# Performance work log

Measured on AMD Instinct MI355X. Metric: run time of the kernel, lower is better.

Reference implementation:

```python
import jax, jax.numpy as jnp
import numpy as np
import math

H = 8
D_MODEL = 32
D_HEAD = 4
FACTOR = 5
EPS = 1e-5

DATANUM = 1024
B = 512            # outer batch; becomes attention sequence length
C = 32
L = DATANUM // 8   # 128; becomes attention batch
U = min(FACTOR * int(math.ceil(math.log(B))), B)  # 35 (U_part == u since L_Q == L_K == B)


def setup_inputs() -> dict:
    key = jax.random.key(0)
    ks = jax.random.split(key, 16)
    s = 0.05
    return {
        'x': jax.random.normal(ks[0], (B, C, L), jnp.float32),
        'Wq': jax.random.normal(ks[1], (D_MODEL, D_MODEL), jnp.float32) * s,
        'bq': jnp.zeros((D_MODEL,), jnp.float32),
        'Wk': jax.random.normal(ks[2], (D_MODEL, D_MODEL), jnp.float32) * s,
        'bk': jnp.zeros((D_MODEL,), jnp.float32),
        'Wv': jax.random.normal(ks[3], (D_MODEL, D_MODEL), jnp.float32) * s,
        'bv': jnp.zeros((D_MODEL,), jnp.float32),
        'Wo': jax.random.normal(ks[4], (D_MODEL, D_MODEL), jnp.float32) * s,
        'bo': jnp.zeros((D_MODEL,), jnp.float32),
        'bn1_gamma': jnp.ones((C,), jnp.float32),
        'bn1_beta': jnp.zeros((C,), jnp.float32),
        'bn1_mean': jnp.zeros((C,), jnp.float32),
        'bn1_var': jnp.ones((C,), jnp.float32),
        'W1': jax.random.normal(ks[5], (DATANUM * 8, DATANUM * 4), jnp.float32) * 0.01,
        'b1': jnp.zeros((DATANUM * 8,), jnp.float32),
        'W2': jax.random.normal(ks[6], (DATANUM * 4, DATANUM * 8), jnp.float32) * 0.01,
        'b2': jnp.zeros((DATANUM * 4,), jnp.float32),
        'bn2_gamma': jnp.ones((C,), jnp.float32),
        'bn2_beta': jnp.zeros((C,), jnp.float32),
        'bn2_mean': jnp.zeros((C,), jnp.float32),
        'bn2_var': jnp.ones((C,), jnp.float32),
        'index_sample': jax.random.randint(ks[7], (B, U), 0, B, jnp.int64),
    }


def _bn(x, gamma, beta, mean, var):
    # eval-mode BatchNorm1d over channel dim of (batch, C, length)
    inv = jax.lax.rsqrt(var + EPS)
    return (x - mean[None, :, None]) * (inv * gamma)[None, :, None] + beta[None, :, None]


def _prob_attention(Q, K, V, index_sample):
    # Q,K,V: (Ba, H, Lq, D) self-attention, Lq == Lk. Informer ProbAttention, mask_flag=True.
    Ba, Hh, Lq, D = Q.shape
    u = index_sample.shape[1]
    # sparsity measurement on sampled keys
    K_sample = K[:, :, index_sample, :]                       # (Ba,H,Lq,U,D)
    QK_sample = jnp.einsum('bhld,bhlud->bhlu', Q, K_sample)
    M = QK_sample.max(axis=-1) - QK_sample.sum(axis=-1) / Lq  # (Ba,H,Lq)
    _, M_top = jax.lax.top_k(M, u)                            # (Ba,H,u) selected queries
    Q_reduce = jnp.take_along_axis(Q, M_top[..., None], axis=2)  # (Ba,H,u,D)
    scores = jnp.einsum('bhud,bhkd->bhuk', Q_reduce, K) / jnp.sqrt(jnp.float32(D))
    # ProbMask: causal w.r.t. the selected query's original position
    causal = jnp.arange(Lq)[None, None, None, :] > M_top[..., None]
    scores = jnp.where(causal, -jnp.inf, scores)
    attn = jax.nn.softmax(scores, axis=-1)
    upd = jnp.einsum('bhuk,bhkd->bhud', attn, V)              # (Ba,H,u,D)
    context = jnp.cumsum(V, axis=2)                           # initial context (mask_flag=True)
    b_idx = jnp.arange(Ba)[:, None, None]
    h_idx = jnp.arange(Hh)[None, :, None]
    context = context.at[b_idx, h_idx, M_top].set(upd)
    return context


def reference(x, Wq, bq, Wk, bk, Wv, bv, Wo, bo,
              bn1_gamma, bn1_beta, bn1_mean, bn1_var,
              W1, b1, W2, b2,
              bn2_gamma, bn2_beta, bn2_mean, bn2_var,
              index_sample):
    Bsz, Cc, Ll = x.shape
    res1 = x
    xa = jnp.transpose(x, (2, 0, 1))                          # (L, B, 32): attn batch=L, seq=B

    def heads(t):
        return jnp.transpose(t.reshape(Ll, Bsz, H, D_HEAD), (0, 2, 1, 3))

    Q = heads(xa @ Wq.T + bq)
    K = heads(xa @ Wk.T + bk)
    V = heads(xa @ Wv.T + bv)
    ctx = _prob_attention(Q, K, V, index_sample)              # (L,H,B,D)
    out = jnp.transpose(ctx, (0, 2, 1, 3)).reshape(Ll, Bsz, D_MODEL)
    out = out @ Wo.T + bo
    xh = jax.nn.relu(out)                                     # dropout = identity (eval)
    xh = jnp.transpose(xh, (1, 2, 0))                         # (B,32,L)
    xh = _bn(xh + res1, bn1_gamma, bn1_beta, bn1_mean, bn1_var)
    res2 = xh
    f = xh.reshape(Bsz, Cc * Ll)
    f = jax.nn.relu(f @ W1.T + b1)
    f = jax.nn.relu(f @ W2.T + b2)
    f = f.reshape(Bsz, Cc, Ll)
    return _bn(f + res2, bn2_gamma, bn2_beta, bn2_mean, bn2_var)
```

## Files before the change

### kernel.cpp

```cpp
#include <hip/hip_runtime.h>
#include <stdint.h>

#define EPSF 1e-5f
#define NEG_INF (-1e30f)

typedef float f32x4 __attribute__((ext_vector_type(4)));
typedef __bf16 bf16x8 __attribute__((ext_vector_type(8)));
typedef unsigned short u16x8 __attribute__((ext_vector_type(8)));

typedef __attribute__((address_space(3))) unsigned char* as3_ptr;
typedef const __attribute__((address_space(1))) unsigned char* as1_ptr;

__device__ __forceinline__ void async16(const void* g, void* l) {
  __builtin_amdgcn_global_load_lds((as1_ptr)g, (as3_ptr)l, 16, 0, 0);
}

__device__ __forceinline__ unsigned short f2bf(float f) {
  union { float f; unsigned int u; } v; v.f = f;
  unsigned int r = v.u + 0x7FFFu + ((v.u >> 16) & 1u);
  return (unsigned short)(r >> 16);
}
__device__ __forceinline__ unsigned short f2bf_fast(float f) {
  union { float f; unsigned int u; } v; v.f = f;
  return (unsigned short)((v.u + 0x8000u) >> 16);
}

__global__ __launch_bounds__(256) void transpose_k(const float* __restrict__ src,
                                                   float* __restrict__ dst, int R, int C) {
  __shared__ float tl[32][33];
  int tx = threadIdx.x & 31, ty = threadIdx.x >> 5;
  int c0 = blockIdx.x * 32, r0 = blockIdx.y * 32;
#pragma unroll
  for (int i = 0; i < 4; i++)
    tl[ty + i * 8][tx] = src[(size_t)(r0 + ty + i * 8) * C + c0 + tx];
  __syncthreads();
#pragma unroll
  for (int i = 0; i < 4; i++)
    dst[(size_t)(c0 + ty + i * 8) * R + r0 + tx] = tl[tx][ty + i * 8];
}

__global__ __launch_bounds__(256) void qkv_k(const float* __restrict__ xT,
    const float* __restrict__ Wq, const float* __restrict__ bq,
    const float* __restrict__ Wk, const float* __restrict__ bk,
    const float* __restrict__ Wv, const float* __restrict__ bv,
    float* __restrict__ Q, float* __restrict__ Kq, float* __restrict__ Vq) {
  __shared__ float xs[64 * 33];
  __shared__ float wq[32 * 33], wk[32 * 33], wvs[32 * 33];
  __shared__ float bqs[32], bks[32], bvs[32];
  int tid = threadIdx.x;
  int a = blockIdx.x;
  int tbase = blockIdx.y * 256;
#pragma unroll
  for (int i = 0; i < 4; i++) {
    int e = i * 256 + tid; int r = e >> 5, c = e & 31;
    wq[r * 33 + c] = Wq[e]; wk[r * 33 + c] = Wk[e]; wvs[r * 33 + c] = Wv[e];
  }
  if (tid < 32) { bqs[tid] = bq[tid]; bks[tid] = bk[tid]; bvs[tid] = bv[tid]; }
  int tl = tid & 63, rg = tid >> 6;
  for (int ch = 0; ch < 4; ch++) {
    __syncthreads();
#pragma unroll
    for (int i = 0; i < 8; i++) {
      int e = i * 256 + tid; int r = e >> 5, c = e & 31;
      xs[r * 33 + c] = xT[(size_t)a * 16384 + (size_t)(tbase + ch * 64) * 32 + e];
    }
    __syncthreads();
    float qa[8], ka[8], va[8];
#pragma unroll
    for (int r8 = 0; r8 < 8; r8++) {
      int r = rg * 8 + r8; qa[r8] = bqs[r]; ka[r8] = bks[r]; va[r8] = bvs[r];
    }
    for (int c = 0; c < 32; c++) {
      float xv = xs[tl * 33 + c];
#pragma unroll
      for (int r8 = 0; r8 < 8; r8++) {
        int r = rg * 8 + r8;
        qa[r8] += xv * wq[r * 33 + c];
        ka[r8] += xv * wk[r * 33 + c];
        va[r8] += xv * wvs[r * 33 + c];
      }
    }
    int t = tbase + ch * 64 + tl;
#pragma unroll
    for (int r8 = 0; r8 < 8; r8++) {
      int r = rg * 8 + r8;
      size_t o = (size_t)a * 16384 + (size_t)r * 512 + t;
      Q[o] = qa[r8]; Kq[o] = ka[r8]; Vq[o] = va[r8];
    }
  }
}

__global__ __launch_bounds__(512) void topk_k(const float* __restrict__ Q,
    const float* __restrict__ Kq, const int* __restrict__ idxs,
    int* __restrict__ Mtop, int U) {
  __shared__ float Ks[2048];
  __shared__ float Ml[512];
  __shared__ float rv[8];
  __shared__ int ri[8];
  int bh = blockIdx.x;
  int tid = threadIdx.x, lane = tid & 63, wv = tid >> 6;
  size_t base = (size_t)bh * 2048;
#pragma unroll
  for (int i = 0; i < 4; i++) Ks[i * 512 + tid] = Kq[base + i * 512 + tid];
  float q0 = Q[base + tid], q1 = Q[base + 512 + tid];
  float q2 = Q[base + 1024 + tid], q3 = Q[base + 1536 + tid];
  __syncthreads();
  float mx = NEG_INF, sm = 0.f;
  for (int u = 0; u < U; u++) {
    int it = idxs[tid * U + u];
    it = min(max(it, 0), 511);
    float s = q0 * Ks[it] + q1 * Ks[512 + it] + q2 * Ks[1024 + it] + q3 * Ks[1536 + it];
    mx = fmaxf(mx, s); sm += s;
  }
  Ml[tid] = mx - sm * (1.f / 512.f);
  __syncthreads();
  for (int s_i = 0; s_i < U; s_i++) {
    float v = Ml[tid]; int ii = tid;
#pragma unroll
    for (int off = 32; off; off >>= 1) {
      float ov = __shfl_xor(v, off); int oi = __shfl_xor(ii, off);
      if (ov > v || (ov == v && oi < ii)) { v = ov; ii = oi; }
    }
    if (lane == 0) { rv[wv] = v; ri[wv] = ii; }
    __syncthreads();
    if (tid == 0) {
      float bv = rv[0]; int bi = ri[0];
      for (int w = 1; w < 8; w++)
        if (rv[w] > bv || (rv[w] == bv && ri[w] < bi)) { bv = rv[w]; bi = ri[w]; }
      Mtop[bh * U + s_i] = bi;
      Ml[bi] = NEG_INF;
    }
    __syncthreads();
  }
}

__global__ __launch_bounds__(256) void attn_k(const float* __restrict__ Q,
    const float* __restrict__ Kq, const float* __restrict__ Vq,
    const int* __restrict__ Mtop, float* __restrict__ Ctx, int U) {
  __shared__ float Ks[2048];
  __shared__ float Vs[2048];
  __shared__ int mt[64];
  __shared__ float Qr[64][4];
  __shared__ float upd[64][4];
  int bh = blockIdx.x;
  int tid = threadIdx.x, lane = tid & 63, wv = tid >> 6;
  size_t base = (size_t)bh * 2048;
#pragma unroll
  for (int i = 0; i < 8; i++) {
    Ks[i * 256 + tid] = Kq[base + i * 256 + tid];
    Vs[i * 256 + tid] = Vq[base + i * 256 + tid];
  }
  if (tid < U) mt[tid] = Mtop[bh * U + tid];
  __syncthreads();
  if (tid < 4 * U) { int u = tid >> 2, d = tid & 3; Qr[u][d] = Q[base + d * 512 + mt[u]]; }
  __syncthreads();
  for (int u = wv; u < U; u += 4) {
    int mrow = mt[u];
    float q0 = Qr[u][0], q1 = Qr[u][1], q2 = Qr[u][2], q3 = Qr[u][3];
    float sv[8]; float lmax = NEG_INF;
#pragma unroll
    for (int jj = 0; jj < 8; jj++) {
      int k = jj * 64 + lane;
      float s = NEG_INF;
      if (k <= mrow)
        s = 0.5f * (q0 * Ks[k] + q1 * Ks[512 + k] + q2 * Ks[1024 + k] + q3 * Ks[1536 + k]);
      sv[jj] = s; lmax = fmaxf(lmax, s);
    }
#pragma unroll
    for (int off = 32; off; off >>= 1) lmax = fmaxf(lmax, __shfl_xor(lmax, off));
    float ls = 0.f, p0 = 0.f, p1 = 0.f, p2 = 0.f, p3 = 0.f;
#pragma unroll
    for (int jj = 0; jj < 8; jj++) {
      int k = jj * 64 + lane;
      if (k <= mrow) {
        float p = __expf(sv[jj] - lmax);
        ls += p; p0 += p * Vs[k]; p1 += p * Vs[512 + k];
        p2 += p * Vs[1024 + k]; p3 += p * Vs[1536 + k];
      }
    }
#pragma unroll
    for (int off = 32; off; off >>= 1) {
      ls += __shfl_xor(ls, off); p0 += __shfl_xor(p0, off); p1 += __shfl_xor(p1, off);
      p2 += __shfl_xor(p2, off); p3 += __shfl_xor(p3, off);
    }
    if (lane == 0) {
      float inv = 1.f / ls;
      upd[u][0] = p0 * inv; upd[u][1] = p1 * inv; upd[u][2] = p2 * inv; upd[u][3] = p3 * inv;
    }
  }
  __syncthreads();
  {
    float v[8];
    int b0 = wv * 512 + lane * 8;
#pragma unroll
    for (int q = 0; q < 8; q++) v[q] = Vs[b0 + q];
#pragma unroll
    for (int q = 1; q < 8; q++) v[q] += v[q - 1];
    float x = v[7];
    for (int off = 1; off < 64; off <<= 1) {
      float y = __shfl_up(x, off);
      if (lane >= off) x += y;
    }
    float excl = x - v[7];
#pragma unroll
    for (int q = 0; q < 8; q++) Vs[b0 + q] = v[q] + excl;
  }
  __syncthreads();
  if (tid < 4 * U) { int u = tid >> 2, d = tid & 3; Vs[d * 512 + mt[u]] = upd[u][d]; }
  __syncthreads();
#pragma unroll
  for (int i = 0; i < 8; i++) Ctx[base + i * 256 + tid] = Vs[i * 256 + tid];
}

__global__ __launch_bounds__(256) void oproj_k(const float* __restrict__ Ctx,
    const float* __restrict__ Wo, const float* __restrict__ bo, float* __restrict__ Y) {
  __shared__ float cs[32 * 256];
  __shared__ float wo[32 * 33];
  __shared__ float bos[32];
  int tid = threadIdx.x;
  int a = blockIdx.x, t0 = blockIdx.y * 256;
#pragma unroll
  for (int i = 0; i < 4; i++) {
    int e = i * 256 + tid; int r = e >> 5, c = e & 31;
    wo[r * 33 + c] = Wo[e];
  }
  if (tid < 32) bos[tid] = bo[tid];
#pragma unroll
  for (int i = 0; i < 32; i++) {
    int e = i * 256 + tid; int row = e >> 8, col = e & 255;
    cs[e] = Ctx[(size_t)a * 16384 + (size_t)row * 512 + t0 + col];
  }
  __syncthreads();
  int rl = tid & 31, tw = tid >> 5;
  for (int ti = 0; ti < 32; ti++) {
    int t = ti * 8 + tw;
    float acc = bos[rl];
#pragma unroll
    for (int rp = 0; rp < 32; rp++) acc += cs[rp * 256 + t] * wo[rl * 33 + rp];
    Y[(size_t)a * 16384 + (size_t)(t0 + t) * 32 + rl] = acc;
  }
}

__global__ __launch_bounds__(256) void bn1t_k(const float* __restrict__ Y,
    const float* __restrict__ x, const float* __restrict__ g1, const float* __restrict__ be1,
    const float* __restrict__ me1, const float* __restrict__ va1,
    float* __restrict__ Xh, unsigned short* __restrict__ Fb) {
  __shared__ float tl[32][33];
  int tx = threadIdx.x & 31, ty = threadIdx.x >> 5;
  int c0 = blockIdx.x * 32;
  int r0 = blockIdx.y * 32;
#pragma unroll
  for (int i = 0; i < 4; i++)
    tl[ty + i * 8][tx] = Y[(size_t)(r0 + ty + i * 8) * 16384 + c0 + tx];
  __syncthreads();
#pragma unroll
  for (int i = 0; i < 4; i++) {
    int m = c0 + ty + i * 8;
    int a = r0 + tx;
    float v = tl[tx][ty + i * 8];
    int ch = m & 31;
    size_t oi = (size_t)m * 128 + a;
    float val = fmaxf(v, 0.f) + x[oi];
    float s = g1[ch] * rsqrtf(va1[ch] + EPSF);
    float res = (val - me1[ch]) * s + be1[ch];
    Xh[oi] = res;
    Fb[oi] = f2bf(res);
  }
}

template <int MI, int NJ, int EPI>
__global__ __launch_bounds__(256) void gemm_ps(
    const unsigned short* __restrict__ A, const float* __restrict__ Bw,
    const float* __restrict__ bias, int K, int N, int MT, int NPX, int SPLITK,
    float* __restrict__ Pout, int M,
    unsigned short* __restrict__ Hout, const float* __restrict__ res2,
    const float* __restrict__ g2, const float* __restrict__ be2,
    const float* __restrict__ me2, const float* __restrict__ va2,
    float* __restrict__ Out) {
  constexpr int BM = MI * 32;
  constexpr int BN = NJ * 32;
  constexpr int ABYTES = BM * 32 * 2;
  constexpr int BBYTES = BN * 32 * 4;
  constexpr int SA = ABYTES / 4096;
  constexpr int SB = BBYTES / 4096;
  __shared__ unsigned char lds[ABYTES + BBYTES];

  int tid = threadIdx.x;
  int lane = tid & 63, wv = tid >> 6;
  int wm = wv >> 1, wn = wv & 1;
  int lin = blockIdx.x;
  int xcd = lin & 7, slot = lin >> 3;
  int tilesPerSp = MT * NPX;
  int sp = slot / tilesPerSp;
  int rem = slot % tilesPerSp;
  int mt = rem % MT;
  int nt = xcd * NPX + rem / MT;
  int m0 = mt * BM + wm * (BM / 2);
  int n0 = nt * BN + wn * (BN / 2);
  int frow = lane & 15, q = lane >> 4;

  int nk = K / (32 * SPLITK);
  int kbase = sp * (K / SPLITK);

  f32x4 acc[MI][NJ];
#pragma unroll
  for (int i = 0; i < MI; i++)
#pragma unroll
    for (int j = 0; j < NJ; j++) { f32x4 z = {0.f, 0.f, 0.f, 0.f}; acc[i][j] = z; }

  int mtile0 = mt * BM;
  int ntile0 = nt * BN;

  for (int k = 0; k < nk; k++) {
    int ks = kbase + k * 32;
#pragma unroll
    for (int i = 0; i < SA; i++) {
      int e = i * 256 + tid;
      int row = e >> 2;
      int g = (e & 3) ^ ((row >> 1) & 3);
      async16(A + (size_t)(mtile0 + row) * K + ks + g * 8, lds + i * 4096 + wv * 1024);
    }
#pragma unroll
    for (int i = 0; i < SB; i++) {
      int e = i * 256 + tid;
      int row = e >> 3;
      int g = (e & 7) ^ (row & 7);
      async16(Bw + (size_t)(ntile0 + row) * K + ks + g * 4,
              lds + ABYTES + i * 4096 + wv * 1024);
    }
    __syncthreads();
    bf16x8 af[MI];
    bf16x8 bfr[NJ];
#pragma unroll
    for (int i = 0; i < MI; i++) {
      int row = wm * (BM / 2) + i * 16 + frow;
      af[i] = *(const bf16x8*)(lds + row * 64 + ((q ^ ((row >> 1) & 3)) << 4));
    }
#pragma unroll
    for (int j = 0; j < NJ; j++) {
      int row = wn * (BN / 2) + j * 16 + frow;
      const unsigned char* rb = lds + ABYTES + row * 128;
      int sw = row & 7;
      float4 w0 = *(const float4*)(rb + (((2 * q + 0) ^ sw) << 4));
      float4 w1 = *(const float4*)(rb + (((2 * q + 1) ^ sw) << 4));
      union { u16x8 u; bf16x8 b; } cv;
      cv.u[0] = f2bf_fast(w0.x); cv.u[1] = f2bf_fast(w0.y);
      cv.u[2] = f2bf_fast(w0.z); cv.u[3] = f2bf_fast(w0.w);
      cv.u[4] = f2bf_fast(w1.x); cv.u[5] = f2bf_fast(w1.y);
      cv.u[6] = f2bf_fast(w1.z); cv.u[7] = f2bf_fast(w1.w);
      bfr[j] = cv.b;
    }
#pragma unroll
    for (int i = 0; i < MI; i++)
#pragma unroll
      for (int j = 0; j < NJ; j++)
        acc[i][j] = __builtin_amdgcn_mfma_f32_16x16x32_bf16(af[i], bfr[j], acc[i][j], 0, 0, 0);
    __syncthreads();
  }

#pragma unroll
  for (int i = 0; i < MI; i++)
#pragma unroll
    for (int j = 0; j < NJ; j++) {
      int n = n0 + j * 16 + frow;
      int mb = m0 + i * 16 + (q << 2);
      if constexpr (EPI == 2) {
        float* pb = Pout + (size_t)sp * M * N;
#pragma unroll
        for (int r = 0; r < 4; r++)
          pb[(size_t)(mb + r) * N + n] = acc[i][j][r];
      } else if constexpr (EPI == 0) {
        float bb = bias[n];
#pragma unroll
        for (int r = 0; r < 4; r++) {
          float v = fmaxf(acc[i][j][r] + bb, 0.f);
          Hout[(size_t)(mb + r) * N + n] = f2bf(v);
        }
      } else {
        float bb = bias[n];
        int ch = n >> 7;
        float s = g2[ch] * rsqrtf(va2[ch] + EPSF);
        float mu = me2[ch], bt = be2[ch];
#pragma unroll
        for (int r = 0; r < 4; r++) {
          float v = fmaxf(acc[i][j][r] + bb, 0.f);
          size_t oi = (size_t)(mb + r) * N + n;
          v += res2[oi];
          Out[oi] = (v - mu) * s + bt;
        }
      }
    }
}

__global__ __launch_bounds__(256) void red1_k(const float* __restrict__ P,
    const float* __restrict__ bias, unsigned short* __restrict__ H, int N, int MN) {
  int idx = blockIdx.x * 256 + threadIdx.x;
  const float4* p = (const float4*)P;
  float4 a = p[idx];
  float4 b = p[idx + (MN >> 2)];
  int n = (idx << 2) & (N - 1);
  float4 bb = *(const float4*)(bias + n);
  ushort4 o;
  o.x = f2bf(fmaxf(a.x + b.x + bb.x, 0.f));
  o.y = f2bf(fmaxf(a.y + b.y + bb.y, 0.f));
  o.z = f2bf(fmaxf(a.z + b.z + bb.z, 0.f));
  o.w = f2bf(fmaxf(a.w + b.w + bb.w, 0.f));
  ((ushort4*)H)[idx] = o;
}

__global__ __launch_bounds__(256) void red2_k(const float* __restrict__ P,
    const float* __restrict__ bias, const float* __restrict__ Xh,
    const float* __restrict__ g2, const float* __restrict__ be2,
    const float* __restrict__ me2, const float* __restrict__ va2,
    float* __restrict__ Out, int N, int MN) {
  int idx = blockIdx.x * 256 + threadIdx.x;
  const float4* p = (const float4*)P;
  int mn4 = MN >> 2;
  float4 a = p[idx], b = p[idx + mn4], c = p[idx + 2 * mn4], d = p[idx + 3 * mn4];
  int n = (idx << 2) & (N - 1);
  int ch = n >> 7;
  float4 bb = *(const float4*)(bias + n);
  float4 xh = ((const float4*)Xh)[idx];
  float s = g2[ch] * rsqrtf(va2[ch] + EPSF);
  float mu = me2[ch], bt = be2[ch];
  float4 o;
  o.x = (fmaxf(a.x + b.x + c.x + d.x + bb.x, 0.f) + xh.x - mu) * s + bt;
  o.y = (fmaxf(a.y + b.y + c.y + d.y + bb.y, 0.f) + xh.y - mu) * s + bt;
  o.z = (fmaxf(a.z + b.z + c.z + d.z + bb.z, 0.f) + xh.z - mu) * s + bt;
  o.w = (fmaxf(a.w + b.w + c.w + d.w + bb.w, 0.f) + xh.w - mu) * s + bt;
  ((float4*)Out)[idx] = o;
}

extern "C" void kernel_launch(void* const* d_in, const int* in_sizes, int n_in,
                              void* d_out, int out_size, void* d_ws, size_t ws_size,
                              hipStream_t stream) {
  const float* x  = (const float*)d_in[0];
  const float* Wq = (const float*)d_in[1];  const float* bq = (const float*)d_in[2];
  const float* Wk = (const float*)d_in[3];  const float* bk = (const float*)d_in[4];
  const float* Wv = (const float*)d_in[5];  const float* bv = (const float*)d_in[6];
  const float* Wo = (const float*)d_in[7];  const float* bo = (const float*)d_in[8];
  const float* g1 = (const float*)d_in[9];  const float* be1 = (const float*)d_in[10];
  const float* me1 = (const float*)d_in[11]; const float* va1 = (const float*)d_in[12];
  const float* W1 = (const float*)d_in[13]; const float* b1 = (const float*)d_in[14];
  const float* W2 = (const float*)d_in[15]; const float* b2 = (const float*)d_in[16];
  const float* g2 = (const float*)d_in[17]; const float* be2 = (const float*)d_in[18];
  const float* me2 = (const float*)d_in[19]; const float* va2 = (const float*)d_in[20];
  const int* idxs = (const int*)d_in[21];
  int U = in_sizes[21] / 512;
  float* out = (float*)d_out;

  char* ws = (char*)d_ws;
  float* QC = (float*)(ws);
  float* Kb = (float*)(ws + (8u << 20));
  float* Vb = (float*)(ws + (16u << 20));
  float* YT = (float*)(ws + (24u << 20));
  float* Xh = (float*)(ws + (32u << 20));
  int* Mtop = (int*)(ws + (40u << 20));
  float* P1 = (float*)(ws + (48u << 20));
  float* P2 = (float*)(ws + (80u << 20));
  unsigned short* Fb = (unsigned short*)Vb;
  unsigned short* Hb = (unsigned short*)Kb;
  bool splitk = ws_size >= (size_t)(112u) * (1u << 20);

  dim3 b256(256);
  transpose_k<<<dim3(4, 512), b256, 0, stream>>>(x, YT, 16384, 128);
  qkv_k<<<dim3(128, 2), b256, 0, stream>>>(YT, Wq, bq, Wk, bk, Wv, bv, QC, Kb, Vb);
  topk_k<<<dim3(1024), dim3(512), 0, stream>>>(QC, Kb, idxs, Mtop, U);
  attn_k<<<dim3(1024), b256, 0, stream>>>(QC, Kb, Vb, Mtop, QC, U);
  oproj_k<<<dim3(128, 2), b256, 0, stream>>>(QC, Wo, bo, YT);
  bn1t_k<<<dim3(512, 4), b256, 0, stream>>>(YT, x, g1, be1, me1, va1, Xh, Fb);

  if (splitk) {
    gemm_ps<4, 2, 2><<<dim3(1024), b256, 0, stream>>>(
        Fb, W1, nullptr, 4096, 8192, 4, 16, 2, P1, 512,
        nullptr, nullptr, nullptr, nullptr, nullptr, nullptr, nullptr);
    red1_k<<<dim3(4096), b256, 0, stream>>>(P1, b1, Hb, 8192, 512 * 8192);
    gemm_ps<4, 2, 2><<<dim3(1024), b256, 0, stream>>>(
        Hb, W2, nullptr, 8192, 4096, 4, 8, 4, P2, 512,
        nullptr, nullptr, nullptr, nullptr, nullptr, nullptr, nullptr);
    red2_k<<<dim3(2048), b256, 0, stream>>>(P2, b2, Xh, g2, be2, me2, va2, out,
                                            4096, 512 * 4096);
  } else {
    gemm_ps<4, 2, 0><<<dim3(512), b256, 0, stream>>>(
        Fb, W1, b1, 4096, 8192, 4, 16, 1, nullptr, 512,
        Hb, nullptr, nullptr, nullptr, nullptr, nullptr, nullptr);
    gemm_ps<4, 2, 1><<<dim3(256), b256, 0, stream>>>(
        Hb, W2, b2, 8192, 4096, 4, 8, 1, nullptr, 512,
        nullptr, Xh, g2, be2, me2, va2, out);
  }
}
```

Baseline: 630.3 us.

## Pre-convert FFN weights to bf16 and use larger-tile split-K GEMM

```diff
diff --git a/kernel.cpp b/kernel.cpp
--- a/kernel.cpp
+++ b/kernel.cpp
@@ -266,6 +266,94 @@
     Xh[oi] = res;
     Fb[oi] = f2bf(res);
   }
+}
+
+__global__ __launch_bounds__(256) void wcvt_k(const float* __restrict__ W,
+    unsigned short* __restrict__ Wb, int n4) {
+  int stride = gridDim.x * 256;
+  for (int idx = blockIdx.x * 256 + threadIdx.x; idx < n4; idx += stride) {
+    float4 w = ((const float4*)W)[idx];
+    ushort4 o;
+    o.x = f2bf(w.x); o.y = f2bf(w.y); o.z = f2bf(w.z); o.w = f2bf(w.w);
+    ((ushort4*)Wb)[idx] = o;
+  }
+}
+
+__global__ __launch_bounds__(256, 3) void gemm_bf(
+    const unsigned short* __restrict__ A, const unsigned short* __restrict__ B,
+    int K, int N, int MT, int NPX, int SPLITK, float* __restrict__ P, int M) {
+  __shared__ unsigned char lds[16384];
+  int tid = threadIdx.x;
+  int lane = tid & 63, wv = tid >> 6;
+  int wm = wv >> 1, wn = wv & 1;
+  int lin = blockIdx.x;
+  int xcd = lin & 7, slot = lin >> 3;
+  int tilesPerSp = MT * NPX;
+  int sp = slot / tilesPerSp;
+  int rem = slot % tilesPerSp;
+  int mt = rem % MT;
+  int nt = xcd * NPX + rem / MT;
+  int mtile0 = mt * 128, ntile0 = nt * 128;
+  int m0 = mtile0 + wm * 64, n0 = ntile0 + wn * 64;
+  int frow = lane & 15, q = lane >> 4;
+
+  int nk = K / (32 * SPLITK);
+  int kbase = sp * (K / SPLITK);
+
+  f32x4 acc[4][4];
+#pragma unroll
+  for (int i = 0; i < 4; i++)
+#pragma unroll
+    for (int j = 0; j < 4; j++) { f32x4 z = {0.f, 0.f, 0.f, 0.f}; acc[i][j] = z; }
+
+  for (int k = 0; k < nk; k++) {
+    int ks = kbase + k * 32;
+#pragma unroll
+    for (int i = 0; i < 2; i++) {
+      int e = i * 256 + tid;
+      int row = e >> 2;
+      int g = (e & 3) ^ ((row >> 1) & 3);
+      async16(A + (size_t)(mtile0 + row) * K + ks + g * 8, lds + i * 4096 + wv * 1024);
+    }
+#pragma unroll
+    for (int i = 0; i < 2; i++) {
+      int e = i * 256 + tid;
+      int row = e >> 2;
+      int g = (e & 3) ^ ((row >> 1) & 3);
+      async16(B + (size_t)(ntile0 + row) * K + ks + g * 8,
+              lds + 8192 + i * 4096 + wv * 1024);
+    }
+    __syncthreads();
+    bf16x8 af[4], bfr[4];
+#pragma unroll
+    for (int i = 0; i < 4; i++) {
+      int row = wm * 64 + i * 16 + frow;
+      af[i] = *(const bf16x8*)(lds + row * 64 + ((q ^ ((row >> 1) & 3)) << 4));
+    }
+#pragma unroll
+    for (int j = 0; j < 4; j++) {
+      int row = wn * 64 + j * 16 + frow;
+      bfr[j] = *(const bf16x8*)(lds + 8192 + row * 64 + ((q ^ ((row >> 1) & 3)) << 4));
+    }
+#pragma unroll
+    for (int i = 0; i < 4; i++)
+#pragma unroll
+      for (int j = 0; j < 4; j++)
+        acc[i][j] = __builtin_amdgcn_mfma_f32_16x16x32_bf16(af[i], bfr[j], acc[i][j], 0, 0, 0);
+    __syncthreads();
+  }
+
+  float* pb = P + (size_t)sp * M * N;
+#pragma unroll
+  for (int i = 0; i < 4; i++)
+#pragma unroll
+    for (int j = 0; j < 4; j++) {
+      int n = n0 + j * 16 + frow;
+      int mb = m0 + i * 16 + (q << 2);
+#pragma unroll
+      for (int r = 0; r < 4; r++)
+        pb[(size_t)(mb + r) * N + n] = acc[i][j][r];
+    }
 }
 
 template <int MI, int NJ, int EPI>
@@ -284,7 +372,6 @@
   constexpr int SA = ABYTES / 4096;
   constexpr int SB = BBYTES / 4096;
   __shared__ unsigned char lds[ABYTES + BBYTES];
-
   int tid = threadIdx.x;
   int lane = tid & 63, wv = tid >> 6;
   int wm = wv >> 1, wn = wv & 1;
@@ -298,19 +385,14 @@
   int m0 = mt * BM + wm * (BM / 2);
   int n0 = nt * BN + wn * (BN / 2);
   int frow = lane & 15, q = lane >> 4;
-
   int nk = K / (32 * SPLITK);
   int kbase = sp * (K / SPLITK);
-
   f32x4 acc[MI][NJ];
 #pragma unroll
   for (int i = 0; i < MI; i++)
 #pragma unroll
     for (int j = 0; j < NJ; j++) { f32x4 z = {0.f, 0.f, 0.f, 0.f}; acc[i][j] = z; }
-
-  int mtile0 = mt * BM;
-  int ntile0 = nt * BN;
-
+  int mtile0 = mt * BM, ntile0 = nt * BN;
   for (int k = 0; k < nk; k++) {
     int ks = kbase + k * 32;
 #pragma unroll
@@ -357,7 +439,6 @@
         acc[i][j] = __builtin_amdgcn_mfma_f32_16x16x32_bf16(af[i], bfr[j], acc[i][j], 0, 0, 0);
     __syncthreads();
   }
-
 #pragma unroll
   for (int i = 0; i < MI; i++)
 #pragma unroll
@@ -392,43 +473,41 @@
     }
 }
 
-__global__ __launch_bounds__(256) void red1_k(const float* __restrict__ P,
-    const float* __restrict__ bias, unsigned short* __restrict__ H, int N, int MN) {
-  int idx = blockIdx.x * 256 + threadIdx.x;
-  const float4* p = (const float4*)P;
-  float4 a = p[idx];
-  float4 b = p[idx + (MN >> 2)];
-  int n = (idx << 2) & (N - 1);
-  float4 bb = *(const float4*)(bias + n);
-  ushort4 o;
-  o.x = f2bf(fmaxf(a.x + b.x + bb.x, 0.f));
-  o.y = f2bf(fmaxf(a.y + b.y + bb.y, 0.f));
-  o.z = f2bf(fmaxf(a.z + b.z + bb.z, 0.f));
-  o.w = f2bf(fmaxf(a.w + b.w + bb.w, 0.f));
-  ((ushort4*)H)[idx] = o;
-}
-
-__global__ __launch_bounds__(256) void red2_k(const float* __restrict__ P,
+template <int EPI>
+__global__ __launch_bounds__(256) void red_k(const float* __restrict__ P, int SP,
     const float* __restrict__ bias, const float* __restrict__ Xh,
     const float* __restrict__ g2, const float* __restrict__ be2,
     const float* __restrict__ me2, const float* __restrict__ va2,
-    float* __restrict__ Out, int N, int MN) {
+    unsigned short* __restrict__ H, float* __restrict__ Out, int N, int MN) {
   int idx = blockIdx.x * 256 + threadIdx.x;
   const float4* p = (const float4*)P;
   int mn4 = MN >> 2;
-  float4 a = p[idx], b = p[idx + mn4], c = p[idx + 2 * mn4], d = p[idx + 3 * mn4];
+  float4 s = p[idx];
+  for (int sp = 1; sp < SP; sp++) {
+    float4 t = p[idx + (size_t)sp * mn4];
+    s.x += t.x; s.y += t.y; s.z += t.z; s.w += t.w;
+  }
   int n = (idx << 2) & (N - 1);
-  int ch = n >> 7;
   float4 bb = *(const float4*)(bias + n);
-  float4 xh = ((const float4*)Xh)[idx];
-  float s = g2[ch] * rsqrtf(va2[ch] + EPSF);
-  float mu = me2[ch], bt = be2[ch];
-  float4 o;
-  o.x = (fmaxf(a.x + b.x + c.x + d.x + bb.x, 0.f) + xh.x - mu) * s + bt;
-  o.y = (fmaxf(a.y + b.y + c.y + d.y + bb.y, 0.f) + xh.y - mu) * s + bt;
-  o.z = (fmaxf(a.z + b.z + c.z + d.z + bb.z, 0.f) + xh.z - mu) * s + bt;
-  o.w = (fmaxf(a.w + b.w + c.w + d.w + bb.w, 0.f) + xh.w - mu) * s + bt;
-  ((float4*)Out)[idx] = o;
+  if constexpr (EPI == 0) {
+    ushort4 o;
+    o.x = f2bf(fmaxf(s.x + bb.x, 0.f));
+    o.y = f2bf(fmaxf(s.y + bb.y, 0.f));
+    o.z = f2bf(fmaxf(s.z + bb.z, 0.f));
+    o.w = f2bf(fmaxf(s.w + bb.w, 0.f));
+    ((ushort4*)H)[idx] = o;
+  } else {
+    int ch = n >> 7;
+    float sc = g2[ch] * rsqrtf(va2[ch] + EPSF);
+    float mu = me2[ch], bt = be2[ch];
+    float4 xh = ((const float4*)Xh)[idx];
+    float4 o;
+    o.x = (fmaxf(s.x + bb.x, 0.f) + xh.x - mu) * sc + bt;
+    o.y = (fmaxf(s.y + bb.y, 0.f) + xh.y - mu) * sc + bt;
+    o.z = (fmaxf(s.z + bb.z, 0.f) + xh.z - mu) * sc + bt;
+    o.w = (fmaxf(s.w + bb.w, 0.f) + xh.w - mu) * sc + bt;
+    ((float4*)Out)[idx] = o;
+  }
 }
 
 extern "C" void kernel_launch(void* const* d_in, const int* in_sizes, int n_in,
@@ -456,11 +535,14 @@
   float* YT = (float*)(ws + (24u << 20));
   float* Xh = (float*)(ws + (32u << 20));
   int* Mtop = (int*)(ws + (40u << 20));
+  unsigned short* Fb = (unsigned short*)Vb;
+  unsigned short* Hb = (unsigned short*)Kb;
+  unsigned short* Wb = (unsigned short*)(ws + (48u << 20));
+  float* PA = (float*)(ws + (112u << 20));
   float* P1 = (float*)(ws + (48u << 20));
   float* P2 = (float*)(ws + (80u << 20));
-  unsigned short* Fb = (unsigned short*)Vb;
-  unsigned short* Hb = (unsigned short*)Kb;
-  bool splitk = ws_size >= (size_t)(112u) * (1u << 20);
+  bool tierA = ws_size >= (size_t)176 * (1u << 20);
+  bool tierB = !tierA && ws_size >= (size_t)112 * (1u << 20);
 
   dim3 b256(256);
   transpose_k<<<dim3(4, 512), b256, 0, stream>>>(x, YT, 16384, 128);
@@ -470,16 +552,28 @@
   oproj_k<<<dim3(128, 2), b256, 0, stream>>>(QC, Wo, bo, YT);
   bn1t_k<<<dim3(512, 4), b256, 0, stream>>>(YT, x, g1, be1, me1, va1, Xh, Fb);
 
-  if (splitk) {
+  if (tierA) {
+    wcvt_k<<<dim3(2048), b256, 0, stream>>>(W1, Wb, (8192 * 4096) / 4);
+    gemm_bf<<<dim3(1024), b256, 0, stream>>>(Fb, Wb, 4096, 8192, 4, 8, 4, PA, 512);
+    red_k<0><<<dim3(4096), b256, 0, stream>>>(PA, 4, b1, nullptr, nullptr, nullptr,
+                                              nullptr, nullptr, Hb, nullptr, 8192,
+                                              512 * 8192);
+    wcvt_k<<<dim3(2048), b256, 0, stream>>>(W2, Wb, (4096 * 8192) / 4);
+    gemm_bf<<<dim3(1024), b256, 0, stream>>>(Hb, Wb, 8192, 4096, 4, 4, 8, PA, 512);
+    red_k<1><<<dim3(2048), b256, 0, stream>>>(PA, 8, b2, Xh, g2, be2, me2, va2,
+                                              nullptr, out, 4096, 512 * 4096);
+  } else if (tierB) {
     gemm_ps<4, 2, 2><<<dim3(1024), b256, 0, stream>>>(
         Fb, W1, nullptr, 4096, 8192, 4, 16, 2, P1, 512,
         nullptr, nullptr, nullptr, nullptr, nullptr, nullptr, nullptr);
-    red1_k<<<dim3(4096), b256, 0, stream>>>(P1, b1, Hb, 8192, 512 * 8192);
+    red_k<0><<<dim3(4096), b256, 0, stream>>>(P1, 2, b1, nullptr, nullptr, nullptr,
+                                              nullptr, nullptr, Hb, nullptr, 8192,
+                                              512 * 8192);
     gemm_ps<4, 2, 2><<<dim3(1024), b256, 0, stream>>>(
         Hb, W2, nullptr, 8192, 4096, 4, 8, 4, P2, 512,
         nullptr, nullptr, nullptr, nullptr, nullptr, nullptr, nullptr);
-    red2_k<<<dim3(2048), b256, 0, stream>>>(P2, b2, Xh, g2, be2, me2, va2, out,
-                                            4096, 512 * 4096);
+    red_k<1><<<dim3(2048), b256, 0, stream>>>(P2, 4, b2, Xh, g2, be2, me2, va2,
+                                              nullptr, out, 4096, 512 * 4096);
   } else {
     gemm_ps<4, 2, 0><<<dim3(512), b256, 0, stream>>>(
         Fb, W1, b1, 4096, 8192, 4, 16, 1, nullptr, 512,
```

Measured after the change: 590.0 us. 1.07x faster.
